# Kernel optimization log

Hardware: AMD Instinct MI355X
Metric: run time of the kernel (lower is better)

Reference implementation:

```python
import jax, jax.numpy as jnp
import numpy as np

NUM_HEAD = 8


def setup_inputs() -> dict:
    key = jax.random.key(0)
    ks = jax.random.split(key, 4)
    B, nd, nh, nw, N, C = 1, 4, 4, 4, 512, 512
    x = jax.random.normal(ks[0], (B, nd, nh, nw, N, C), dtype=jnp.float32)
    w_qkv = jax.random.normal(ks[1], (C, 3 * C), dtype=jnp.float32) / np.sqrt(C).astype(np.float32)
    b_qkv = jnp.zeros((3 * C,), dtype=jnp.float32)
    w_proj = jax.random.normal(ks[2], (C, C), dtype=jnp.float32) / np.sqrt(C).astype(np.float32)
    b_proj = jnp.zeros((C,), dtype=jnp.float32)
    return {"x": x, "w_qkv": w_qkv, "b_qkv": b_qkv, "w_proj": w_proj, "b_proj": b_proj}


def reference(x, w_qkv, b_qkv, w_proj, b_proj):
    B, nd, nh, nw, N, C = x.shape
    hd = C // NUM_HEAD
    # QKV projection, split into q/k/v with per-head layout [B,nd,nh,nw,N,H,hd]
    qkv = (x @ w_qkv + b_qkv).reshape(B, nd, nh, nw, N, 3, NUM_HEAD, hd)
    q = qkv[..., 0, :, :]
    k = qkv[..., 1, :, :]
    v = qkv[..., 2, :, :]
    # Block-local attention. NOTE: original module defines self.scale but never
    # applies it in forward, so no 1/sqrt(hd) scaling here (faithful to source).
    attn = jnp.einsum('...qhd,...khd->...hqk', q, k)  # [B,nd,nh,nw,H,N,N]
    attn = jax.nn.softmax(attn, axis=-1)
    out = jnp.einsum('...hqk,...khd->...qhd', attn, v)  # [B,nd,nh,nw,N,H,hd]
    out = out.reshape(B, nd, nh, nw, N, C)
    return out @ w_proj + b_proj
```

## Files before the change

### kernel.cpp

```cpp
#include <hip/hip_runtime.h>
#include <hip/hip_bf16.h>

typedef _Float16 half8_t __attribute__((ext_vector_type(8)));
typedef _Float16 half4_t __attribute__((ext_vector_type(4)));
typedef _Float16 half2_t __attribute__((ext_vector_type(2)));
typedef float    f32x4   __attribute__((ext_vector_type(4)));
typedef float    f32x16  __attribute__((ext_vector_type(16)));

#define CDIM 512
#define NHEAD 8
#define HD 64
#define NTOK 512
#define NWIN 64
#define TC 1536

__device__ __forceinline__ float fexp2(float x) {
  float r;
  asm("v_exp_f32 %0, %1" : "=v"(r) : "v"(x));
  return r;
}

#define GLL16(g, l)                                                        \
  __builtin_amdgcn_global_load_lds((const __attribute__((address_space(1))) void*)(g), \
                                   (__attribute__((address_space(3))) void*)(l), 16, 0, 0)


__global__ __launch_bounds__(256) void cvt_x(const float* __restrict__ x,
                                             _Float16* __restrict__ x16, int n8) {
  int i = blockIdx.x * 256 + threadIdx.x;
  if (i < n8) {
    float4 v0 = *(const float4*)(x + (size_t)i * 8);
    float4 v1 = *(const float4*)(x + (size_t)i * 8 + 4);
    half8_t h = {(_Float16)v0.x, (_Float16)v0.y, (_Float16)v0.z, (_Float16)v0.w,
                 (_Float16)v1.x, (_Float16)v1.y, (_Float16)v1.z, (_Float16)v1.w};
    *(half8_t*)(x16 + (size_t)i * 8) = h;
  }
}

__global__ __launch_bounds__(256) void prep_weights(
    const float* __restrict__ wqkv, const float* __restrict__ wproj,
    _Float16* __restrict__ wqkvT, _Float16* __restrict__ wprojT) {
  __shared__ _Float16 T[64 * 65];
  int b = blockIdx.x;
  const float* src; _Float16* dst; int Cc, r0, c0;
  if (b < 192) {
    src = wqkv; dst = wqkvT; Cc = 1536;
    c0 = (b % 24) * 64; r0 = (b / 24) * 64;
  } else {
    b -= 192; src = wproj; dst = wprojT; Cc = 512;
    c0 = (b & 7) * 64; r0 = (b >> 3) * 64;
  }
  const int t = threadIdx.x;
#pragma unroll
  for (int i = 0; i < 16; ++i) {
    int idx = i * 256 + t, rr = idx >> 6, cc = idx & 63;
    T[rr * 65 + cc] = (_Float16)src[(size_t)(r0 + rr) * Cc + c0 + cc];
  }
  __syncthreads();
#pragma unroll
  for (int i = 0; i < 2; ++i) {
    int idx = i * 256 + t, ol = idx >> 3, c8 = idx & 7;
    half8_t vv;
#pragma unroll
    for (int e = 0; e < 8; ++e) vv[e] = T[(c8 * 8 + e) * 65 + ol];
    *(half8_t*)(dst + (size_t)(c0 + ol) * 512 + r0 + c8 * 8) = vv;
  }
}

__global__ __launch_bounds__(256) void gemm1_qkv(
    const _Float16* __restrict__ x16,
    const _Float16* __restrict__ wT,
    const float* __restrict__ bias,
    _Float16* __restrict__ qkv) {
  __shared__ __align__(16) _Float16 smem[4 * 128 * 64];
  char* base = (char*)smem;
  const int tid = threadIdx.x;
  const int l = tid & 63;
  const int wid = tid >> 6;
  const int wr = wid >> 1, wc = wid & 1;
  const int lr = l & 15, g = l >> 4;
  const int swzf = (lr & 7) << 4;
  const int m0 = blockIdx.x * 128;
  const int cb = blockIdx.y * 128;
  const int j = cb >> 9;

  const int srow = l >> 3;
  const int scol = 16 * ((l & 7) ^ srow);
  const size_t aRowB = (size_t)(m0 + srow) * 1024 + scol;
  const size_t bRowB = (size_t)(cb + srow) * 1024 + scol;

#define STAGE_G1(buf, k0)                                                         \
  {                                                                               \
    char* Ad = base + (buf)*16384 + wid * 4096;                                   \
    char* Bd = base + 32768 + (buf)*16384 + wid * 4096;                           \
    _Pragma("unroll") for (int i = 0; i < 4; ++i) {                               \
      int chunk = wid * 4 + i;                                                    \
      GLL16((const char*)x16 + aRowB + (size_t)chunk * 8192 + (k0)*2, Ad + i * 1024); \
      GLL16((const char*)wT + bRowB + (size_t)chunk * 8192 + (k0)*2, Bd + i * 1024);  \
    }                                                                             \
  }

  STAGE_G1(0, 0);
  __syncthreads();

  f32x4 acc[4][4] = {};
  for (int ks = 0; ks < 8; ++ks) {
    const int cur = ks & 1;
    if (ks < 7) STAGE_G1(cur ^ 1, (ks + 1) * 64);
    char* AsB = base + cur * 16384;
    char* BsB = base + 32768 + cur * 16384;
#pragma unroll
    for (int kk = 0; kk < 2; ++kk) {
      half8_t a[4], b[4];
#pragma unroll
      for (int mt = 0; mt < 4; ++mt) {
        int row = wr * 64 + mt * 16 + lr;
        a[mt] = *(const half8_t*)(AsB + row * 128 + ((kk * 64 + g * 16) ^ swzf));
      }
#pragma unroll
      for (int nt = 0; nt < 4; ++nt) {
        int row = wc * 64 + nt * 16 + lr;
        b[nt] = *(const half8_t*)(BsB + row * 128 + ((kk * 64 + g * 16) ^ swzf));
      }
#pragma unroll
      for (int mt = 0; mt < 4; ++mt)
#pragma unroll
        for (int nt = 0; nt < 4; ++nt)
          acc[mt][nt] = __builtin_amdgcn_mfma_f32_16x16x32_f16(a[mt], b[nt], acc[mt][nt], 0, 0, 0);
    }
    __syncthreads();
  }

  if (j == 2) {
#pragma unroll
    for (int nt = 0; nt < 4; ++nt) {
      const int ch = cb + wc * 64 + nt * 16 + lr;
      const int h = (ch >> 6) & 7, d = ch & 63;
      const float bvs = bias[ch];
#pragma unroll
      for (int mt = 0; mt < 4; ++mt) {
        const int row = m0 + wr * 64 + mt * 16 + g * 4;
        const int wL = row >> 9, n = row & 511;
        _Float16* panel = qkv + ((size_t)(wL * 24 + 16 + h) << 15);
        const int kg = n >> 4, hh = (n >> 2) & 1, e4 = (n & 8) >> 1;
        half4_t pk = {(_Float16)(acc[mt][nt][0] + bvs), (_Float16)(acc[mt][nt][1] + bvs),
                      (_Float16)(acc[mt][nt][2] + bvs), (_Float16)(acc[mt][nt][3] + bvs)};
        *(half4_t*)(panel + ((size_t)(kg * 2 + hh) * 64 + d) * 8 + e4) = pk;
      }
    }
  } else {
    const float scl = (j == 0) ? 1.44269504f : 1.0f;
    char* CB = base;
#pragma unroll
    for (int nt = 0; nt < 4; ++nt) {
      const int chl = wc * 64 + nt * 16 + lr;
      const float bvs = bias[cb + chl];
#pragma unroll
      for (int mt = 0; mt < 4; ++mt) {
#pragma unroll
        for (int r = 0; r < 4; ++r) {
          int nl = wr * 64 + mt * 16 + g * 4 + r;
          *(_Float16*)(CB + nl * 256 + ((chl * 2) ^ ((nl & 7) << 5))) =
              (_Float16)((acc[mt][nt][r] + bvs) * scl);
        }
      }
    }
    __syncthreads();
#pragma unroll
    for (int i = 0; i < 8; ++i) {
      int idx = i * 256 + tid, nl = idx >> 4, c8 = idx & 15;
      half8_t vv = *(const half8_t*)(CB + nl * 256 + ((c8 * 16) ^ ((nl & 7) << 5)));
      int chg = cb + c8 * 8;
      int h = (chg >> 6) & 7, d = chg & 63;
      int ng = m0 + nl, wL = ng >> 9, nn = ng & 511;
      _Float16* panel = qkv + ((size_t)(wL * 24 + j * 8 + h) << 15);
      *(half8_t*)(panel + (size_t)nn * 64 + d) = vv;
    }
  }
}

__global__ __launch_bounds__(512) void attn_win(_Float16* __restrict__ qkv) {
  __shared__ __align__(16) char ring[4 * 8192];
  char* ringB = ring;
  const int tid = threadIdx.x;
  const int l = tid & 63;
  const int wid = tid >> 6;
  const int q32 = l & 31;
  const int h2 = l >> 5;
  const int wh = blockIdx.x;
  const int qc = blockIdx.y;
  const int h = wh & 7;
  const int w = wh >> 3;
  _Float16* Qp = qkv + ((size_t)(w * 24 + h) << 15);
  const _Float16* Kp = qkv + ((size_t)(w * 24 + 8 + h) << 15);
  const _Float16* Vp = qkv + ((size_t)(w * 24 + 16 + h) << 15);
  const int qrow = qc * 256 + wid * 32 + q32;

  const size_t kSrc = (size_t)(l >> 3) * 128 + (size_t)((l & 7) ^ (l >> 3)) * 16;
  const int kof0 = ((0 * 2 + h2) ^ (q32 & 7)) << 4;
  const int kof1 = ((1 * 2 + h2) ^ (q32 & 7)) << 4;
  const int kof2 = ((2 * 2 + h2) ^ (q32 & 7)) << 4;
  const int kof3 = ((3 * 2 + h2) ^ (q32 & 7)) << 4;
  const int voff = 4096 + h2 * 1024 + q32 * 16;

#define ISSUE_SLOT(KT)                                                            \
  {                                                                               \
    char* sb = ringB + ((KT)&3) * 8192;                                           \
    if (wid < 4) {                                                                \
      GLL16((const char*)Kp + (size_t)(KT)*4096 + (size_t)wid * 1024 + kSrc,      \
            sb + wid * 1024);                                                     \
    } else {                                                                      \
      GLL16((const char*)Vp + (size_t)(KT)*4096 + (size_t)(wid - 4) * 1024 + l * 16, \
            sb + 4096 + (wid - 4) * 1024);                                        \
    }                                                                             \
  }

  half8_t qf[4];
#pragma unroll
  for (int j = 0; j < 4; ++j)
    qf[j] = *(const half8_t*)(Qp + (size_t)qrow * 64 + j * 16 + h2 * 8);
  asm volatile("s_waitcnt vmcnt(0)" ::: "memory");

  ISSUE_SLOT(0) ISSUE_SLOT(1) ISSUE_SLOT(2)

  f32x16 o0 = {}, o1 = {};
  float m_run = -1e30f, lsum = 0.f;

#define AITER(KT, NW)                                                             \
  {                                                                               \
    asm volatile("s_waitcnt vmcnt(" NW ")" ::: "memory");                         \
    __builtin_amdgcn_sched_barrier(0);                                            \
    asm volatile("s_barrier" ::: "memory");                                       \
    if ((KT) + 3 < 16) ISSUE_SLOT((KT) + 3)                                       \
    char* sl = ringB + ((KT)&3) * 8192;                                           \
    half8_t kf0 = *(const half8_t*)(sl + q32 * 128 + kof0);                       \
    half8_t kf1 = *(const half8_t*)(sl + q32 * 128 + kof1);                       \
    half8_t kf2 = *(const half8_t*)(sl + q32 * 128 + kof2);                       \
    half8_t kf3 = *(const half8_t*)(sl + q32 * 128 + kof3);                       \
    __builtin_amdgcn_s_setprio(1);                                                \
    f32x16 s = {};                                                                \
    s = __builtin_amdgcn_mfma_f32_32x32x16_f16(kf0, qf[0], s, 0, 0, 0);           \
    s = __builtin_amdgcn_mfma_f32_32x32x16_f16(kf1, qf[1], s, 0, 0, 0);           \
    s = __builtin_amdgcn_mfma_f32_32x32x16_f16(kf2, qf[2], s, 0, 0, 0);           \
    s = __builtin_amdgcn_mfma_f32_32x32x16_f16(kf3, qf[3], s, 0, 0, 0);           \
    __builtin_amdgcn_s_setprio(0);                                                \
    float ma = fmaxf(fmaxf(s[0], s[1]), s[2]);                                    \
    float mb = fmaxf(fmaxf(s[3], s[4]), s[5]);                                    \
    float mc = fmaxf(fmaxf(s[6], s[7]), s[8]);                                    \
    float md = fmaxf(fmaxf(s[9], s[10]), s[11]);                                  \
    float me = fmaxf(fmaxf(s[12], s[13]), s[14]);                                 \
    float mf_ = fmaxf(fmaxf(ma, mb), mc);                                         \
    float mg = fmaxf(fmaxf(md, me), s[15]);                                       \
    float tmax = fmaxf(mf_, mg);                                                  \
    tmax = fmaxf(tmax, __shfl_xor(tmax, 32));                                     \
    if (!__all(tmax <= m_run + 11.5f)) {                                          \
      float mNew = fmaxf(m_run, tmax);                                            \
      float sc = fexp2(m_run - mNew);                                             \
      lsum *= sc;                                                                 \
      _Pragma("unroll") for (int r = 0; r < 16; ++r) { o0[r] *= sc; o1[r] *= sc; }\
      m_run = mNew;                                                               \
    }                                                                             \
    half8_t pf0, pf1;                                                             \
    float tsum = 0.f;                                                             \
    _Pragma("unroll") for (int e = 0; e < 4; ++e) {                               \
      float a0 = fexp2(s[2 * e] - m_run), a1 = fexp2(s[2 * e + 1] - m_run);       \
      tsum += a0 + a1;                                                            \
      ((half2_t*)&pf0)[e] =                                                       \
          __builtin_bit_cast(half2_t, __builtin_amdgcn_cvt_pkrtz(a0, a1));        \
    }                                                                             \
    _Pragma("unroll") for (int e = 0; e < 4; ++e) {                               \
      float a0 = fexp2(s[8 + 2 * e] - m_run), a1 = fexp2(s[9 + 2 * e] - m_run);   \
      tsum += a0 + a1;                                                            \
      ((half2_t*)&pf1)[e] =                                                       \
          __builtin_bit_cast(half2_t, __builtin_amdgcn_cvt_pkrtz(a0, a1));        \
    }                                                                             \
    tsum += __shfl_xor(tsum, 32);                                                 \
    lsum += tsum;                                                                 \
    half8_t vf0 = *(const half8_t*)(sl + voff);                                   \
    half8_t vf1 = *(const half8_t*)(sl + voff + 512);                             \
    half8_t vf2 = *(const half8_t*)(sl + voff + 2048);                            \
    half8_t vf3 = *(const half8_t*)(sl + voff + 2560);                            \
    __builtin_amdgcn_s_setprio(1);                                                \
    o0 = __builtin_amdgcn_mfma_f32_32x32x16_f16(vf0, pf0, o0, 0, 0, 0);           \
    o1 = __builtin_amdgcn_mfma_f32_32x32x16_f16(vf1, pf0, o1, 0, 0, 0);           \
    o0 = __builtin_amdgcn_mfma_f32_32x32x16_f16(vf2, pf1, o0, 0, 0, 0);           \
    o1 = __builtin_amdgcn_mfma_f32_32x32x16_f16(vf3, pf1, o1, 0, 0, 0);           \
    __builtin_amdgcn_s_setprio(0);                                                \
  }

  AITER(0, "2")  AITER(1, "2")  AITER(2, "2")  AITER(3, "2")
  AITER(4, "2")  AITER(5, "2")  AITER(6, "2")  AITER(7, "2")
  AITER(8, "2")  AITER(9, "2")  AITER(10, "2") AITER(11, "2")
  AITER(12, "2") AITER(13, "2") AITER(14, "1") AITER(15, "0")

  const float inv = 1.0f / lsum;
#pragma unroll
  for (int rq = 0; rq < 4; ++rq) {
    half4_t v0, v1;
#pragma unroll
    for (int i = 0; i < 4; ++i) {
      v0[i] = (_Float16)(o0[rq * 4 + i] * inv);
      v1[i] = (_Float16)(o1[rq * 4 + i] * inv);
    }
    *(half4_t*)(Qp + (size_t)qrow * 64 + 8 * rq + 4 * h2) = v0;
    *(half4_t*)(Qp + (size_t)qrow * 64 + 32 + 8 * rq + 4 * h2) = v1;
  }
}

__global__ __launch_bounds__(256) void gemm2_proj(
    const _Float16* __restrict__ qkv,
    const _Float16* __restrict__ wpT,
    const float* __restrict__ bias,
    float* __restrict__ out) {
  const int tid = threadIdx.x, l = tid & 63;
  const int wid = tid >> 6, wr = wid >> 1, wc = wid & 1;
  const int lr = l & 15, lk8 = (l >> 4) * 8;
  const int m0 = blockIdx.x * 128, n0 = blockIdx.y * 128;
  size_t aBase[4];
#pragma unroll
  for (int mt = 0; mt < 4; ++mt) {
    int row = m0 + wr * 64 + mt * 16 + lr;
    int wL = row >> 9, n = row & 511;
    aBase[mt] = ((size_t)(wL * 24) << 15) + (size_t)n * 64 + lk8;
  }
  size_t bBase[4];
#pragma unroll
  for (int nt = 0; nt < 4; ++nt)
    bBase[nt] = (size_t)(n0 + wc * 64 + nt * 16 + lr) * 512 + lk8;

  half8_t a[4], b[4];
#pragma unroll
  for (int mt = 0; mt < 4; ++mt) a[mt] = *(const half8_t*)(qkv + aBase[mt]);
#pragma unroll
  for (int nt = 0; nt < 4; ++nt) b[nt] = *(const half8_t*)(wpT + bBase[nt]);

  f32x4 acc[4][4] = {};
#pragma unroll 2
  for (int ks = 0; ks < 16; ++ks) {
    half8_t an[4], bn[4];
    if (ks < 15) {
      const size_t aoff = (size_t)((ks + 1) >> 1) * 32768 + (size_t)((ks + 1) & 1) * 32;
#pragma unroll
      for (int mt = 0; mt < 4; ++mt) an[mt] = *(const half8_t*)(qkv + aBase[mt] + aoff);
#pragma unroll
      for (int nt = 0; nt < 4; ++nt) bn[nt] = *(const half8_t*)(wpT + bBase[nt] + (ks + 1) * 32);
    }
#pragma unroll
    for (int mt = 0; mt < 4; ++mt)
#pragma unroll
      for (int nt = 0; nt < 4; ++nt)
        acc[mt][nt] = __builtin_amdgcn_mfma_f32_16x16x32_f16(a[mt], b[nt], acc[mt][nt], 0, 0, 0);
#pragma unroll
    for (int i = 0; i < 4; ++i) { a[i] = an[i]; b[i] = bn[i]; }
  }
#pragma unroll
  for (int nt = 0; nt < 4; ++nt) {
    int col = n0 + wc * 64 + nt * 16 + lr;
    float bv = bias[col];
#pragma unroll
    for (int mt = 0; mt < 4; ++mt) {
      int row = m0 + wr * 64 + mt * 16 + ((l >> 4) << 2);
#pragma unroll
      for (int r = 0; r < 4; ++r)
        out[(size_t)(row + r) * 512 + col] = acc[mt][nt][r] + bv;
    }
  }
}

extern "C" void kernel_launch(void* const* d_in, const int* in_sizes, int n_in,
                              void* d_out, int out_size, void* d_ws, size_t ws_size,
                              hipStream_t stream) {
  const float* x = (const float*)d_in[0];
  const float* wqkv = (const float*)d_in[1];
  const float* bqkv = (const float*)d_in[2];
  const float* wproj = (const float*)d_in[3];
  const float* bproj = (const float*)d_in[4];
  float* out = (float*)d_out;

  _Float16* wqkvT = (_Float16*)d_ws;
  _Float16* wprojT = wqkvT + (size_t)TC * CDIM;
  _Float16* chunkws = wprojT + (size_t)CDIM * CDIM;
  const size_t fixed = ((size_t)TC * CDIM + (size_t)CDIM * CDIM) * sizeof(_Float16);
  const size_t perwin = ((size_t)NTOK * CDIM + (size_t)24 * 32768) * sizeof(_Float16);
  int nw = 64;
  while (nw > 1 && fixed + (size_t)nw * perwin > ws_size) nw >>= 1;

  prep_weights<<<dim3(256), 256, 0, stream>>>(wqkv, wproj, wqkvT, wprojT);
  for (int wbase = 0; wbase < NWIN; wbase += nw) {
    const float* xc = x + (size_t)wbase * NTOK * CDIM;
    float* oc = out + (size_t)wbase * NTOK * CDIM;
    _Float16* x16 = chunkws;
    _Float16* qkvws = chunkws + (size_t)nw * NTOK * CDIM;
    const int n8 = nw * NTOK * CDIM / 8;
    cvt_x<<<dim3((n8 + 255) / 256), 256, 0, stream>>>(xc, x16, n8);
    gemm1_qkv<<<dim3(nw * 4, 12), 256, 0, stream>>>(x16, wqkvT, bqkv, qkvws);
    attn_win<<<dim3(nw * 8, 2), 512, 0, stream>>>(qkvws);
    gemm2_proj<<<dim3(nw * 4, 4), 256, 0, stream>>>(qkvws, wprojT, bproj, oc);
  }
}
```

Baseline: 222.4 us.

## Enlarge QKV GEMM tiles to 256x256 with a 4-stage LDS ring pipeline

The QKV projection GEMM moves from 128x128 tiles with 4 waves and a double buffer to 256x256 tiles with 8 waves. It uses a 4-deep LDS ring of 32-wide K slices, prefetched 3 steps ahead and synchronised with explicit vmcnt waits and raw barriers. MFMA sections run at raised priority. The aim is more data reuse per LDS load and better hiding of global load latency. In exchange it uses more LDS (128 KB) and launches fewer blocks (768 instead of 3072), which may hurt occupancy.

```diff
diff --git a/kernel.cpp b/kernel.cpp
--- a/kernel.cpp
+++ b/kernel.cpp
@@ -67,69 +67,69 @@
   }
 }
 
-__global__ __launch_bounds__(256) void gemm1_qkv(
+__global__ __launch_bounds__(512, 2) void gemm1_qkv(
     const _Float16* __restrict__ x16,
     const _Float16* __restrict__ wT,
     const float* __restrict__ bias,
     _Float16* __restrict__ qkv) {
-  __shared__ __align__(16) _Float16 smem[4 * 128 * 64];
-  char* base = (char*)smem;
+  __shared__ __align__(16) char ring[4 * 32768];
+  char* ringB = ring;
   const int tid = threadIdx.x;
   const int l = tid & 63;
   const int wid = tid >> 6;
-  const int wr = wid >> 1, wc = wid & 1;
+  const int wr = wid >> 2, wc = wid & 3;
   const int lr = l & 15, g = l >> 4;
-  const int swzf = (lr & 7) << 4;
-  const int m0 = blockIdx.x * 128;
-  const int cb = blockIdx.y * 128;
+  const int koff = ((g ^ (lr & 3)) << 4);
+  const int m0 = blockIdx.x * 256;
+  const int cb = blockIdx.y * 256;
   const int j = cb >> 9;
 
-  const int srow = l >> 3;
-  const int scol = 16 * ((l & 7) ^ srow);
-  const size_t aRowB = (size_t)(m0 + srow) * 1024 + scol;
-  const size_t bRowB = (size_t)(cb + srow) * 1024 + scol;
-
-#define STAGE_G1(buf, k0)                                                         \
+  const int srow4 = l >> 2;
+  const int schk = (l & 3) ^ (srow4 & 3);
+  const size_t aSrc = (size_t)(m0 + wid * 32 + srow4) * 1024 + ((size_t)schk << 4);
+  const size_t bSrc = (size_t)(cb + wid * 32 + srow4) * 1024 + ((size_t)schk << 4);
+
+#define ISSUE_G1(KS)                                                              \
   {                                                                               \
-    char* Ad = base + (buf)*16384 + wid * 4096;                                   \
-    char* Bd = base + 32768 + (buf)*16384 + wid * 4096;                           \
-    _Pragma("unroll") for (int i = 0; i < 4; ++i) {                               \
-      int chunk = wid * 4 + i;                                                    \
-      GLL16((const char*)x16 + aRowB + (size_t)chunk * 8192 + (k0)*2, Ad + i * 1024); \
-      GLL16((const char*)wT + bRowB + (size_t)chunk * 8192 + (k0)*2, Bd + i * 1024);  \
+    char* sa = ringB + ((KS)&3) * 32768;                                          \
+    char* sb = sa + 16384;                                                        \
+    _Pragma("unroll") for (int i = 0; i < 2; ++i) {                               \
+      GLL16((const char*)x16 + aSrc + (size_t)i * 16384 + (size_t)(KS)*64,        \
+            sa + wid * 2048 + i * 1024);                                          \
+      GLL16((const char*)wT + bSrc + (size_t)i * 16384 + (size_t)(KS)*64,         \
+            sb + wid * 2048 + i * 1024);                                          \
     }                                                                             \
   }
 
-  STAGE_G1(0, 0);
-  __syncthreads();
-
-  f32x4 acc[4][4] = {};
-  for (int ks = 0; ks < 8; ++ks) {
-    const int cur = ks & 1;
-    if (ks < 7) STAGE_G1(cur ^ 1, (ks + 1) * 64);
-    char* AsB = base + cur * 16384;
-    char* BsB = base + 32768 + cur * 16384;
-#pragma unroll
-    for (int kk = 0; kk < 2; ++kk) {
-      half8_t a[4], b[4];
-#pragma unroll
-      for (int mt = 0; mt < 4; ++mt) {
-        int row = wr * 64 + mt * 16 + lr;
-        a[mt] = *(const half8_t*)(AsB + row * 128 + ((kk * 64 + g * 16) ^ swzf));
-      }
-#pragma unroll
-      for (int nt = 0; nt < 4; ++nt) {
-        int row = wc * 64 + nt * 16 + lr;
-        b[nt] = *(const half8_t*)(BsB + row * 128 + ((kk * 64 + g * 16) ^ swzf));
-      }
-#pragma unroll
-      for (int mt = 0; mt < 4; ++mt)
-#pragma unroll
-        for (int nt = 0; nt < 4; ++nt)
-          acc[mt][nt] = __builtin_amdgcn_mfma_f32_16x16x32_f16(a[mt], b[nt], acc[mt][nt], 0, 0, 0);
-    }
-    __syncthreads();
-  }
+  ISSUE_G1(0) ISSUE_G1(1) ISSUE_G1(2)
+
+  f32x4 acc[8][4] = {};
+
+#define GITER(KS, NW)                                                             \
+  {                                                                               \
+    asm volatile("s_waitcnt vmcnt(" NW ")" ::: "memory");                         \
+    __builtin_amdgcn_sched_barrier(0);                                            \
+    asm volatile("s_barrier" ::: "memory");                                       \
+    if ((KS) + 3 < 16) ISSUE_G1((KS) + 3)                                         \
+    char* sa = ringB + ((KS)&3) * 32768;                                          \
+    char* sb = sa + 16384;                                                        \
+    half8_t a[8], b[4];                                                           \
+    _Pragma("unroll") for (int mt = 0; mt < 8; ++mt)                              \
+        a[mt] = *(const half8_t*)(sa + (wr * 128 + mt * 16 + lr) * 64 + koff);    \
+    _Pragma("unroll") for (int nt = 0; nt < 4; ++nt)                              \
+        b[nt] = *(const half8_t*)(sb + (wc * 64 + nt * 16 + lr) * 64 + koff);     \
+    __builtin_amdgcn_s_setprio(1);                                                \
+    _Pragma("unroll") for (int mt = 0; mt < 8; ++mt)                              \
+        _Pragma("unroll") for (int nt = 0; nt < 4; ++nt)                          \
+            acc[mt][nt] =                                                         \
+                __builtin_amdgcn_mfma_f32_16x16x32_f16(a[mt], b[nt], acc[mt][nt], 0, 0, 0); \
+    __builtin_amdgcn_s_setprio(0);                                                \
+  }
+
+  GITER(0, "8")  GITER(1, "8")  GITER(2, "8")  GITER(3, "8")
+  GITER(4, "8")  GITER(5, "8")  GITER(6, "8")  GITER(7, "8")
+  GITER(8, "8")  GITER(9, "8")  GITER(10, "8") GITER(11, "8")
+  GITER(12, "8") GITER(13, "8") GITER(14, "4") GITER(15, "0")
 
   if (j == 2) {
 #pragma unroll
@@ -138,8 +138,8 @@
       const int h = (ch >> 6) & 7, d = ch & 63;
       const float bvs = bias[ch];
 #pragma unroll
-      for (int mt = 0; mt < 4; ++mt) {
-        const int row = m0 + wr * 64 + mt * 16 + g * 4;
+      for (int mt = 0; mt < 8; ++mt) {
+        const int row = m0 + wr * 128 + mt * 16 + g * 4;
         const int wL = row >> 9, n = row & 511;
         _Float16* panel = qkv + ((size_t)(wL * 24 + 16 + h) << 15);
         const int kg = n >> 4, hh = (n >> 2) & 1, e4 = (n & 8) >> 1;
@@ -149,27 +149,28 @@
       }
     }
   } else {
+    __syncthreads();
     const float scl = (j == 0) ? 1.44269504f : 1.0f;
-    char* CB = base;
+    char* CB = ringB;
 #pragma unroll
     for (int nt = 0; nt < 4; ++nt) {
       const int chl = wc * 64 + nt * 16 + lr;
       const float bvs = bias[cb + chl];
 #pragma unroll
-      for (int mt = 0; mt < 4; ++mt) {
+      for (int mt = 0; mt < 8; ++mt) {
 #pragma unroll
         for (int r = 0; r < 4; ++r) {
-          int nl = wr * 64 + mt * 16 + g * 4 + r;
-          *(_Float16*)(CB + nl * 256 + ((chl * 2) ^ ((nl & 7) << 5))) =
+          int nl = wr * 128 + mt * 16 + g * 4 + r;
+          *(_Float16*)(CB + nl * 512 + ((chl * 2) ^ ((nl & 7) << 5))) =
               (_Float16)((acc[mt][nt][r] + bvs) * scl);
         }
       }
     }
     __syncthreads();
 #pragma unroll
-    for (int i = 0; i < 8; ++i) {
-      int idx = i * 256 + tid, nl = idx >> 4, c8 = idx & 15;
-      half8_t vv = *(const half8_t*)(CB + nl * 256 + ((c8 * 16) ^ ((nl & 7) << 5)));
+    for (int i = 0; i < 16; ++i) {
+      int idx = i * 512 + tid, nl = idx >> 5, c8 = idx & 31;
+      half8_t vv = *(const half8_t*)(CB + nl * 512 + ((c8 * 16) ^ ((nl & 7) << 5)));
       int chg = cb + c8 * 8;
       int h = (chg >> 6) & 7, d = chg & 63;
       int ng = m0 + nl, wL = ng >> 9, nn = ng & 511;
@@ -393,7 +394,7 @@
     _Float16* qkvws = chunkws + (size_t)nw * NTOK * CDIM;
     const int n8 = nw * NTOK * CDIM / 8;
     cvt_x<<<dim3((n8 + 255) / 256), 256, 0, stream>>>(xc, x16, n8);
-    gemm1_qkv<<<dim3(nw * 4, 12), 256, 0, stream>>>(x16, wqkvT, bqkv, qkvws);
+    gemm1_qkv<<<dim3(nw * 2, 6), 512, 0, stream>>>(x16, wqkvT, bqkv, qkvws);
     attn_win<<<dim3(nw * 8, 2), 512, 0, stream>>>(qkvws);
     gemm2_proj<<<dim3(nw * 4, 4), 256, 0, stream>>>(qkvws, wprojT, bproj, oc);
   }
```

New measurement: 217.0 us. 2.4% less time.
